# Performance work log

Measured on AMD Instinct MI355X. Metric: run time of the kernel, lower is better.

Reference implementation:

```python
import jax, jax.numpy as jnp
import numpy as np

B = 8
SEQ = 8192
D_MODEL = 256
D_STATE = 64
D_CONV = 4
EXPAND = 4
HEADDIM = 64
N_LAYERS = 8
D_INNER = EXPAND * D_MODEL            # 1024
NHEADS = D_INNER // HEADDIM           # 16
CONV_DIM = D_INNER + 2 * D_STATE      # 1152 (ngroups=1)
D_IN_PROJ = 2 * D_INNER + 2 * D_STATE + NHEADS  # 2192


def setup_inputs():
    key = jax.random.key(0)
    ks = jax.random.split(key, 16)
    rn = lambda k, shape, fan: jax.random.normal(k, shape, jnp.float32) / np.float32(np.sqrt(fan))
    inp = {}
    inp["x"] = jax.random.normal(ks[0], (B, 3, SEQ), jnp.float32)
    inp["conv1_w"] = rn(ks[1], (64, 3, 16), 3 * 16)
    inp["conv1_b"] = rn(ks[2], (64,), 64)
    inp["conv2_w"] = rn(ks[3], (D_MODEL, 64, 16), 64 * 16)
    inp["conv2_b"] = rn(ks[4], (D_MODEL,), D_MODEL)
    inp["in_proj_w"] = rn(ks[5], (N_LAYERS, D_IN_PROJ, D_MODEL), D_MODEL)
    inp["dw_conv_w"] = rn(ks[6], (N_LAYERS, CONV_DIM, D_CONV), D_CONV)
    inp["dw_conv_b"] = rn(ks[7], (N_LAYERS, CONV_DIM), D_CONV)
    inp["dt_bias"] = jax.random.normal(ks[8], (N_LAYERS, NHEADS), jnp.float32) * 0.5
    inp["A_log"] = jax.random.uniform(ks[9], (N_LAYERS, NHEADS), jnp.float32, 0.0, 2.0)
    inp["ssm_D"] = jnp.ones((N_LAYERS, NHEADS), jnp.float32)
    inp["rms_w"] = jnp.ones((N_LAYERS, D_INNER), jnp.float32)
    inp["out_proj_w"] = rn(ks[10], (N_LAYERS, D_MODEL, D_INNER), D_INNER)
    inp["ln_w"] = jnp.ones((D_MODEL,), jnp.float32)
    inp["ln_b"] = jnp.zeros((D_MODEL,), jnp.float32)
    inp["reg1_w"] = rn(ks[11], (128, D_MODEL), D_MODEL)
    inp["reg1_b"] = rn(ks[12], (128,), 128)
    inp["reg2_w"] = rn(ks[13], (1, 128), 128)
    inp["reg2_b"] = rn(ks[14], (1,), 128)
    return inp


def _silu(v):
    return v * jax.nn.sigmoid(v)


def _mamba2_layer(u, in_proj_w, dw_w, dw_b, dt_bias, A_log, ssm_D, rms_w, out_proj_w):
    b, l, _ = u.shape
    zxbcdt = u @ in_proj_w.T                               # (b,l,2192)
    z = zxbcdt[..., :D_INNER]
    xBC = zxbcdt[..., D_INNER:D_INNER + CONV_DIM]
    dt = jax.nn.softplus(zxbcdt[..., D_INNER + CONV_DIM:] + dt_bias)   # (b,l,h)
    # causal depthwise conv1d (kernel D_CONV), then SiLU
    pad = jnp.pad(xBC, ((0, 0), (D_CONV - 1, 0), (0, 0)))
    conv = sum(pad[:, k:k + l, :] * dw_w[:, k] for k in range(D_CONV)) + dw_b
    xBC = _silu(conv)
    xh = xBC[..., :D_INNER].reshape(b, l, NHEADS, HEADDIM)  # (b,l,h,p)
    Bm = xBC[..., D_INNER:D_INNER + D_STATE]                # (b,l,n)
    Cm = xBC[..., D_INNER + D_STATE:]                       # (b,l,n)
    dA = jnp.exp(dt * (-jnp.exp(A_log)))                    # (b,l,h)

    def step(h, inp):
        dA_t, dt_t, x_t, B_t, C_t = inp
        h = h * dA_t[:, :, None, None] + (dt_t[:, :, None] * x_t)[..., None] * B_t[:, None, None, :]
        y = jnp.einsum('bhpn,bn->bhp', h, C_t)
        return h, y

    h0 = jnp.zeros((b, NHEADS, HEADDIM, D_STATE), u.dtype)
    xs = (dA.transpose(1, 0, 2), dt.transpose(1, 0, 2),
          xh.transpose(1, 0, 2, 3), Bm.transpose(1, 0, 2), Cm.transpose(1, 0, 2))
    _, ys = jax.lax.scan(step, h0, xs)                      # (l,b,h,p)
    y = ys.transpose(1, 0, 2, 3) + ssm_D[None, None, :, None] * xh
    y = y.reshape(b, l, D_INNER)
    y = y * _silu(z)                                        # gated
    y = y * jax.lax.rsqrt(jnp.mean(y * y, axis=-1, keepdims=True) + 1e-5) * rms_w
    return y @ out_proj_w.T


def reference(x, conv1_w, conv1_b, conv2_w, conv2_b, in_proj_w, dw_conv_w, dw_conv_b,
              dt_bias, A_log, ssm_D, rms_w, out_proj_w, ln_w, ln_b,
              reg1_w, reg1_b, reg2_w, reg2_b):
    dn = ('NCH', 'OIH', 'NCH')
    h = jax.lax.conv_general_dilated(x, conv1_w, (4,), [(6, 6)], dimension_numbers=dn) + conv1_b[None, :, None]
    h = jax.nn.gelu(h, approximate=False)
    h = jax.lax.conv_general_dilated(h, conv2_w, (2,), [(7, 7)], dimension_numbers=dn) + conv2_b[None, :, None]
    h = jax.nn.gelu(h, approximate=False)
    h = h.transpose(0, 2, 1)                                # (b, 1024, d_model)
    for i in range(N_LAYERS):
        h = _mamba2_layer(h, in_proj_w[i], dw_conv_w[i], dw_conv_b[i],
                          dt_bias[i], A_log[i], ssm_D[i], rms_w[i], out_proj_w[i])
    mu = jnp.mean(h, -1, keepdims=True)
    var = jnp.mean((h - mu) ** 2, -1, keepdims=True)
    h = (h - mu) * jax.lax.rsqrt(var + 1e-5) * ln_w + ln_b  # LayerNorm
    pooled = h.mean(1)
    r = jax.nn.gelu(pooled @ reg1_w.T + reg1_b, approximate=False)
    return r @ reg2_w.T + reg2_b                            # (b, 1)
```

## Files before the change

kernel.cpp:

```cpp
#include <hip/hip_runtime.h>
#include <math.h>

#define NB       8
#define SEQ      8192
#define L1OUT    2048
#define LOUT     1024
#define DMODEL   256
#define DINNER   1024
#define NHEADS   16
#define HEADDIM  64
#define DSTATE   64
#define CONVDIM  1152
#define DINPROJ  2192
#define NPADIN   2304
#define NLAYERS  8
#define NCHUNK   16
#define Q        64

#define N_CAST1 (NLAYERS * NPADIN * DMODEL)
#define N_CAST2 (NLAYERS * DMODEL * DINNER)
#define N_CAST3 (DMODEL * 1024)

typedef _Float16 f16;
typedef __attribute__((ext_vector_type(8))) _Float16 f16x8;
typedef __attribute__((ext_vector_type(4))) _Float16 f16x4;
typedef __attribute__((ext_vector_type(4))) float    f32x4;

__device__ __forceinline__ float gelu_f(float v) {
    return 0.5f * v * (1.0f + erff(v * 0.70710678118654752f));
}
__device__ __forceinline__ float silu_f(float v) {
    return v * __builtin_amdgcn_rcpf(1.0f + __expf(-v));
}

__device__ __forceinline__ void gload16(const void* g, void* l) {
    __builtin_amdgcn_global_load_lds(
        (const __attribute__((address_space(1))) unsigned int*)g,
        (__attribute__((address_space(3))) unsigned int*)l, 16, 0, 0);
}

__device__ __forceinline__ int xcd_chunk(int flat, int nblk) {
    return (flat & 7) * (nblk >> 3) + (flat >> 3);
}

__global__ __launch_bounds__(256) void k_castall(const float* __restrict__ w_in,
                                                 const float* __restrict__ w_out,
                                                 const float* __restrict__ w_c2,
                                                 f16* __restrict__ o_in,
                                                 f16* __restrict__ o_out,
                                                 f16* __restrict__ o_c2) {
    int idx = blockIdx.x * 256 + threadIdx.x;
    if (idx < N_CAST1) {
        int c = idx & 255;
        int r = (idx >> 8) % NPADIN;
        int l = idx / (NPADIN * 256);
        float v = (r < DINPROJ) ? w_in[((size_t)l * DINPROJ + r) * 256 + c] : 0.f;
        o_in[idx] = (f16)v;
    } else if (idx < N_CAST1 + N_CAST2) {
        int i = idx - N_CAST1;
        o_out[i] = (f16)w_out[i];
    } else if (idx < N_CAST1 + N_CAST2 + N_CAST3) {
        int i = idx - N_CAST1 - N_CAST2;
        o_c2[i] = (f16)w_c2[i];
    }
}

__global__ __launch_bounds__(256) void k_conv1(const float* __restrict__ x,
                                               const float* __restrict__ w,
                                               const float* __restrict__ bias,
                                               f16* __restrict__ out) {
    int idx = blockIdx.x * 256 + threadIdx.x;
    int u  = idx & 255;
    int co = (idx >> 8) & 63;
    int b  = idx >> 14;
    int xbase = u * 32 - 8;

    float acc[8];
#pragma unroll
    for (int t = 0; t < 8; ++t) acc[t] = bias[co];

#pragma unroll
    for (int ci = 0; ci < 3; ++ci) {
        const float* xp = x + ((size_t)b * 3 + ci) * SEQ;
        float xb[48];
#pragma unroll
        for (int j = 0; j < 12; ++j) {
            int off = xbase + j * 4;
            float4 v;
            if (off >= 0 && off + 3 < SEQ) {
                v = *(const float4*)&xp[off];
            } else {
                v.x = (off + 0 >= 0 && off + 0 < SEQ) ? xp[off + 0] : 0.f;
                v.y = (off + 1 >= 0 && off + 1 < SEQ) ? xp[off + 1] : 0.f;
                v.z = (off + 2 >= 0 && off + 2 < SEQ) ? xp[off + 2] : 0.f;
                v.w = (off + 3 >= 0 && off + 3 < SEQ) ? xp[off + 3] : 0.f;
            }
            xb[j * 4 + 0] = v.x; xb[j * 4 + 1] = v.y;
            xb[j * 4 + 2] = v.z; xb[j * 4 + 3] = v.w;
        }
        const float* wp = w + (co * 3 + ci) * 16;
        float wv[16];
#pragma unroll
        for (int k = 0; k < 16; ++k) wv[k] = wp[k];
#pragma unroll
        for (int t = 0; t < 8; ++t)
#pragma unroll
            for (int k = 0; k < 16; ++k)
                acc[t] = fmaf(xb[t * 4 + k + 2], wv[k], acc[t]);
    }
    f16x8 o;
#pragma unroll
    for (int t = 0; t < 8; ++t) o[t] = (f16)gelu_f(acc[t]);
    *(f16x8*)&out[((size_t)(b * 64 + co)) * L1OUT + u * 8] = o;
}

__global__ __launch_bounds__(256) void k_im2col(const f16* __restrict__ h1,
                                                f16* __restrict__ A) {
    int idx = blockIdx.x * 256 + threadIdx.x;
    int g = idx & 127;
    int row = idx >> 7;
    int t = row & (LOUT - 1);
    int b = row >> 10;
    int ci = g >> 1, k0 = (g & 1) * 8;
    int pos0 = t * 2 + k0 - 7;
    const f16* hp = h1 + ((size_t)(b * 64 + ci)) * L1OUT;
    f16x8 v;
#pragma unroll
    for (int j = 0; j < 8; ++j) {
        int p = pos0 + j;
        v[j] = (p >= 0 && p < L1OUT) ? hp[p] : (f16)0.f;
    }
    *(f16x8*)&A[(size_t)row * 1024 + g * 8] = v;
}

template<int BM, int EPI>
__global__ __launch_bounds__(256) void k_hgemm(const f16* __restrict__ A,
                                               const f16* __restrict__ Bw,
                                               f16* __restrict__ Ch,
                                               int M, int N, int K,
                                               const float* __restrict__ bias,
                                               const float* __restrict__ dt_bias,
                                               const float* __restrict__ A_log,
                                               float* __restrict__ dadt) {
    constexpr int MI = BM / 32;
    __shared__ f16 As[BM * 64];
    __shared__ f16 Bs[128 * 64];
    int tid  = threadIdx.x;
    int lane = tid & 63, wid = tid >> 6;
    int wm = wid >> 1, wn = wid & 1;

    int nbx = gridDim.x;
    int flat = blockIdx.y * nbx + blockIdx.x;
    int logical = xcd_chunk(flat, nbx * gridDim.y);
    int row0 = (logical / nbx) * BM, col0 = (logical % nbx) * 128;
    int lr = lane & 15, kb = lane >> 4;

    f32x4 acc[MI][4];
#pragma unroll
    for (int mi = 0; mi < MI; ++mi)
#pragma unroll
        for (int ni = 0; ni < 4; ++ni)
            acc[mi][ni] = (f32x4){0.f, 0.f, 0.f, 0.f};

    int sr  = tid >> 3;
    int scx = ((tid & 7) ^ (sr & 7)) * 8;
    int rsw = (lr & 7) * 8;

    for (int k0 = 0; k0 < K; k0 += 64) {
        __syncthreads();
#pragma unroll
        for (int is = 0; is < BM / 32; ++is)
            gload16(A + (size_t)(row0 + is * 32 + sr) * K + k0 + scx,
                    &As[is * 2048 + wid * 512]);
#pragma unroll
        for (int is = 0; is < 4; ++is)
            gload16(Bw + (size_t)(col0 + is * 32 + sr) * K + k0 + scx,
                    &Bs[is * 2048 + wid * 512]);
        __syncthreads();

#pragma unroll
        for (int ks = 0; ks < 2; ++ks) {
            int cbase = (ks * 32 + kb * 8) ^ rsw;
            f16x8 a[MI], b[4];
#pragma unroll
            for (int mi = 0; mi < MI; ++mi)
                a[mi] = *reinterpret_cast<const f16x8*>(
                    &As[(wm * (BM / 2) + mi * 16 + lr) * 64 + cbase]);
#pragma unroll
            for (int ni = 0; ni < 4; ++ni)
                b[ni] = *reinterpret_cast<const f16x8*>(
                    &Bs[(wn * 64 + ni * 16 + lr) * 64 + cbase]);
#pragma unroll
            for (int mi = 0; mi < MI; ++mi)
#pragma unroll
                for (int ni = 0; ni < 4; ++ni)
                    acc[mi][ni] = __builtin_amdgcn_mfma_f32_16x16x32_f16(
                        a[mi], b[ni], acc[mi][ni], 0, 0, 0);
        }
    }

#pragma unroll
    for (int mi = 0; mi < MI; ++mi)
#pragma unroll
        for (int ni = 0; ni < 4; ++ni) {
            int ccol = col0 + wn * 64 + ni * 16 + lr;
            if (ccol < N) {
                int rbase = row0 + wm * (BM / 2) + mi * 16 + kb * 4;
                f32x4 v = acc[mi][ni];
#pragma unroll
                for (int r = 0; r < 4; ++r) {
                    float val = v[r];
                    if (EPI == 1) val = gelu_f(val + bias[ccol]);
                    Ch[(size_t)(rbase + r) * N + ccol] = (f16)val;
                    if (EPI == 2 && ccol >= DINNER + CONVDIM) {
                        int hh = ccol - (DINNER + CONVDIM);
                        float raw = val + dt_bias[hh];
                        float dtv = (raw > 20.f) ? raw : log1pf(__expf(raw));
                        float lda = -__expf(A_log[hh]) * dtv;
                        *(float2*)&dadt[(size_t)(rbase + r) * 32 + hh * 2] =
                            make_float2(lda, dtv);
                    }
                }
            }
        }
}

__global__ __launch_bounds__(256) void k_ssd1(const f16* __restrict__ zx16,
                                              const float* __restrict__ dadt,
                                              const float* __restrict__ dw_w,
                                              const float* __restrict__ dw_b,
                                              const float* __restrict__ ssmD,
                                              f16* __restrict__ y1,
                                              f16* __restrict__ Sbuf16,
                                              float* __restrict__ Abuf,
                                              f16* __restrict__ C16) {
    __shared__ f16 Bs[64][72];
    __shared__ f16 Cs[64][72];
    __shared__ float GT[64][68];
    __shared__ f16 Mw[4][64][72];
    __shared__ float2 LaDt[4][64];

    int tid = threadIdx.x, lane = tid & 63, wid = tid >> 6;
    int bid = xcd_chunk(blockIdx.x, NB * NCHUNK * 4);
    int hq = bid & 3, c = (bid >> 2) & 15, b = bid >> 6;
    int h = hq * 4 + wid;
    int lr = lane & 15, kb = lane >> 4;
    f16* Xs = &Mw[0][0][0];

    {
        int sg = tid % 48;
        int ts = tid / 48;
        if (ts < 4) {
            int xc;
            if (sg < 32)      xc = hq * 256 + sg * 8;
            else if (sg < 40) xc = 1024 + (sg - 32) * 8;
            else              xc = 1088 + (sg - 40) * 8;
            int zc = 1024 + xc;
            float4 wv[8];
            float  bv[8];
#pragma unroll
            for (int j = 0; j < 8; ++j) {
                wv[j] = *(const float4*)&dw_w[(xc + j) * 4];
                bv[j] = dw_b[xc + j];
            }
            int l0 = c * 64 + ts * 16;
            const f16* zrow = zx16 + ((size_t)(b * 1024 + l0)) * DINPROJ + zc;
            f16x8 r0, r1, r2, r3;
            f16x8 zz;
#pragma unroll
            for (int j = 0; j < 8; ++j) zz[j] = (f16)0.f;
            r0 = (l0 >= 3) ? *(const f16x8*)(zrow - 3 * DINPROJ) : zz;
            r1 = (l0 >= 2) ? *(const f16x8*)(zrow - 2 * DINPROJ) : zz;
            r2 = (l0 >= 1) ? *(const f16x8*)(zrow - 1 * DINPROJ) : zz;
#pragma unroll
            for (int t = 0; t < 16; ++t) {
                r3 = *(const f16x8*)(zrow + t * DINPROJ);
                f16x8 o;
#pragma unroll
                for (int j = 0; j < 8; ++j) {
                    float s = bv[j];
                    s = fmaf((float)r0[j], wv[j].x, s);
                    s = fmaf((float)r1[j], wv[j].y, s);
                    s = fmaf((float)r2[j], wv[j].z, s);
                    s = fmaf((float)r3[j], wv[j].w, s);
                    o[j] = (f16)silu_f(s);
                }
                int row = ts * 16 + t;
                if (sg < 32) {
                    f16x4 o0 = {o[0], o[1], o[2], o[3]};
                    f16x4 o1 = {o[4], o[5], o[6], o[7]};
                    *(f16x4*)&Xs[row * 260 + sg * 8]     = o0;
                    *(f16x4*)&Xs[row * 260 + sg * 8 + 4] = o1;
                } else if (sg < 40) {
                    *(f16x8*)&Bs[row][(sg - 32) * 8] = o;
                } else {
                    *(f16x8*)&Cs[row][(sg - 40) * 8] = o;
                }
                r0 = r1; r1 = r2; r2 = r3;
            }
        }
    }

    float2 ad = *(const float2*)&dadt[((size_t)(b * 1024 + c * 64 + lane) * 16 + h) * 2];
    float La = ad.x;
#pragma unroll
    for (int o = 1; o < 64; o <<= 1) {
        float v = __shfl_up(La, o);
        if (lane >= o) La += v;
    }
    float dt_own = ad.y;
    float La63 = __shfl(La, 63);
    float w_own = __expf(La63 - La) * dt_own;
    LaDt[wid][lane] = make_float2(La, dt_own);
    float Dh = ssmD[h];
    __syncthreads();

    if (hq == 0) {
        f16* cp = C16 + (((size_t)(b * 16 + c)) << 12);
#pragma unroll
        for (int it = 0; it < 2; ++it) {
            int cid = it * 256 + tid;
            int row = cid >> 3, off = (cid & 7) * 8;
            *(f16x8*)&cp[row * 64 + off] = *(const f16x8*)&Cs[row][off];
        }
    }

    f16x8 xfrag[4][2];
#pragma unroll
    for (int pi = 0; pi < 4; ++pi)
#pragma unroll
        for (int ks = 0; ks < 2; ++ks) {
            f16x8 v;
#pragma unroll
            for (int j = 0; j < 8; ++j)
                v[j] = Xs[(ks * 32 + kb * 8 + j) * 260 + wid * 64 + pi * 16 + lr];
            xfrag[pi][ks] = v;
        }

    {
        int tq = wid & 1, sq = wid >> 1;
        f32x4 g[2][2];
#pragma unroll
        for (int i = 0; i < 2; ++i)
#pragma unroll
            for (int j = 0; j < 2; ++j) g[i][j] = (f32x4){0.f, 0.f, 0.f, 0.f};
#pragma unroll
        for (int ks = 0; ks < 2; ++ks) {
            f16x8 a[2], bb[2];
#pragma unroll
            for (int ti = 0; ti < 2; ++ti)
                a[ti] = *(const f16x8*)&Cs[tq * 32 + ti * 16 + lr][ks * 32 + kb * 8];
#pragma unroll
            for (int si = 0; si < 2; ++si)
                bb[si] = *(const f16x8*)&Bs[sq * 32 + si * 16 + lr][ks * 32 + kb * 8];
#pragma unroll
            for (int ti = 0; ti < 2; ++ti)
#pragma unroll
                for (int si = 0; si < 2; ++si)
                    g[ti][si] = __builtin_amdgcn_mfma_f32_16x16x32_f16(
                        a[ti], bb[si], g[ti][si], 0, 0, 0);
        }
#pragma unroll
        for (int ti = 0; ti < 2; ++ti)
#pragma unroll
            for (int si = 0; si < 2; ++si)
#pragma unroll
                for (int r = 0; r < 4; ++r)
                    GT[sq * 32 + si * 16 + lr][tq * 32 + ti * 16 + kb * 4 + r] = g[ti][si][r];
    }
    __syncthreads();

    {
        f16x8 brow[8];
#pragma unroll
        for (int i = 0; i < 8; ++i) brow[i] = *(const f16x8*)&Bs[lane][i * 8];
#pragma unroll
        for (int i = 0; i < 8; ++i)
#pragma unroll
            for (int j = 0; j < 8; ++j)
                Mw[wid][i * 8 + j][lane] = (f16)((float)brow[i][j] * w_own);
    }
    __builtin_amdgcn_wave_barrier();

    f16x8 sbfrag[4][2];
#pragma unroll
    for (int ni = 0; ni < 4; ++ni)
#pragma unroll
        for (int ks = 0; ks < 2; ++ks)
            sbfrag[ni][ks] = *(const f16x8*)&Mw[wid][ni * 16 + lr][ks * 32 + kb * 8];

    {
        f32x4 accS[4][4];
#pragma unroll
        for (int pi = 0; pi < 4; ++pi)
#pragma unroll
            for (int ni = 0; ni < 4; ++ni) accS[pi][ni] = (f32x4){0.f, 0.f, 0.f, 0.f};
#pragma unroll
        for (int ks = 0; ks < 2; ++ks)
#pragma unroll
            for (int pi = 0; pi < 4; ++pi)
#pragma unroll
                for (int ni = 0; ni < 4; ++ni)
                    accS[pi][ni] = __builtin_amdgcn_mfma_f32_16x16x32_f16(
                        xfrag[pi][ks], sbfrag[ni][ks], accS[pi][ni], 0, 0, 0);
        size_t sbase = ((size_t)((b * 16 + h) * 16 + c)) << 12;
#pragma unroll
        for (int pi = 0; pi < 4; ++pi)
#pragma unroll
            for (int ni = 0; ni < 4; ++ni)
#pragma unroll
                for (int r = 0; r < 4; ++r)
                    Sbuf16[sbase + (size_t)(pi * 16 + kb * 4 + r) * 64 + ni * 16 + lr] =
                        (f16)accS[pi][ni][r];
        if (lane == 0) Abuf[(b * 16 + h) * 16 + c] = __expf(La63);
    }
    __builtin_amdgcn_wave_barrier();

    {
        int t = lane;
        float la_t = La;
#pragma unroll
        for (int s8 = 0; s8 < 8; ++s8) {
            f16x8 mv;
#pragma unroll
            for (int j = 0; j < 8; ++j) {
                int s = s8 * 8 + j;
                float2 ld = LaDt[wid][s];
                float m = (s <= t) ? GT[s][t] * __expf(la_t - ld.x) * ld.y : 0.f;
                if (s == t) m += Dh;
                mv[j] = (f16)m;
            }
            *(f16x8*)&Mw[wid][t][s8 * 8] = mv;
        }
    }
    __builtin_amdgcn_wave_barrier();

    {
        f32x4 accY[4][4];
#pragma unroll
        for (int ti = 0; ti < 4; ++ti)
#pragma unroll
            for (int pi = 0; pi < 4; ++pi) accY[ti][pi] = (f32x4){0.f, 0.f, 0.f, 0.f};
#pragma unroll
        for (int ks = 0; ks < 2; ++ks) {
            f16x8 af[4];
#pragma unroll
            for (int ti = 0; ti < 4; ++ti)
                af[ti] = *(const f16x8*)&Mw[wid][ti * 16 + lr][ks * 32 + kb * 8];
#pragma unroll
            for (int ti = 0; ti < 4; ++ti)
#pragma unroll
                for (int pi = 0; pi < 4; ++pi)
                    accY[ti][pi] = __builtin_amdgcn_mfma_f32_16x16x32_f16(
                        af[ti], xfrag[pi][ks], accY[ti][pi], 0, 0, 0);
        }
        f16* yp = y1 + ((size_t)(b * 1024 + c * 64)) * 1024 + h * 64;
#pragma unroll
        for (int ti = 0; ti < 4; ++ti)
#pragma unroll
            for (int pi = 0; pi < 4; ++pi)
#pragma unroll
                for (int r = 0; r < 4; ++r)
                    yp[(size_t)(ti * 16 + kb * 4 + r) * 1024 + pi * 16 + lr] =
                        (f16)accY[ti][pi][r];
    }
}

__global__ __launch_bounds__(256) void k_ssd2f(const f16* __restrict__ C16,
                                               const f16* __restrict__ Sbuf16,
                                               const float* __restrict__ Abuf,
                                               const float* __restrict__ dadt,
                                               f16* __restrict__ y2) {
    __shared__ f16 Hs[NCHUNK][1024];
    int tid = threadIdx.x, lane = tid & 63, wv = tid >> 6;
    int bid = xcd_chunk(blockIdx.x, NB * NHEADS * 4);
    int ph = bid & 3, h = (bid >> 2) & 15, b = bid >> 6;
    int bh = b * 16 + h;
    int lr = lane & 15, kb = lane >> 4;
    size_t base = ((size_t)bh << 16) + ph * 1024;

    {
        int lp = tid >> 4;
        int n0 = (tid & 15) * 4;
        int dst = lp * 64 + ((((n0 >> 3) ^ (lp & 7))) << 3) + (n0 & 7);
        float Hl[4];
#pragma unroll
        for (int j = 0; j < 4; ++j) Hl[j] = 0.f;
#pragma unroll
        for (int c = 0; c < NCHUNK; ++c) {
            f16x4 o;
#pragma unroll
            for (int j = 0; j < 4; ++j) o[j] = (f16)Hl[j];
            *(f16x4*)&Hs[c][dst] = o;
            float A = Abuf[bh * 16 + c];
            f16x4 s = *(const f16x4*)&Sbuf16[base + (size_t)c * 4096 + lp * 64 + n0];
#pragma unroll
            for (int j = 0; j < 4; ++j)
                Hl[j] = fmaf(Hl[j], A, (float)s[j]);
        }
    }
    __syncthreads();

    const f16* cpb = C16 + ((size_t)b << 16);
#pragma unroll
    for (int i = 0; i < 4; ++i) {
        int c = wv * 4 + i;
        float2 ad = *(const float2*)&dadt[((size_t)(b * 1024 + c * 64 + lane) * 16 + h) * 2];
        float La = ad.x;
#pragma unroll
        for (int o = 1; o < 64; o <<= 1) {
            float v = __shfl_up(La, o);
            if (lane >= o) La += v;
        }

        f16x8 hfrag[2];
#pragma unroll
        for (int ks = 0; ks < 2; ++ks) {
            int cf = (ks * 32 + kb * 8) ^ ((lr & 7) * 8);
            hfrag[ks] = *(const f16x8*)&Hs[c][lr * 64 + cf];
        }

        const f16* cp = cpb + ((size_t)c << 12);
        f32x4 acc[4];
#pragma unroll
        for (int ti = 0; ti < 4; ++ti) acc[ti] = (f32x4){0.f, 0.f, 0.f, 0.f};
#pragma unroll
        for (int ks = 0; ks < 2; ++ks) {
            f16x8 af[4];
#pragma unroll
            for (int ti = 0; ti < 4; ++ti)
                af[ti] = *(const f16x8*)(cp + (ti * 16 + lr) * 64 + ks * 32 + kb * 8);
#pragma unroll
            for (int ti = 0; ti < 4; ++ti)
                acc[ti] = __builtin_amdgcn_mfma_f32_16x16x32_f16(
                    af[ti], hfrag[ks], acc[ti], 0, 0, 0);
        }
        f16* yp = y2 + ((size_t)(b * 1024 + c * 64)) * 1024 + h * 64 + ph * 16;
#pragma unroll
        for (int ti = 0; ti < 4; ++ti)
#pragma unroll
            for (int r = 0; r < 4; ++r) {
                int t = ti * 16 + kb * 4 + r;
                float sc = __expf(__shfl(La, t));
                yp[(size_t)t * 1024 + lr] = (f16)(sc * acc[ti][r]);
            }
    }
}

__global__ __launch_bounds__(256) void k_gate(const f16* __restrict__ zx16,
                                              const float* __restrict__ rmsw,
                                              const f16* __restrict__ y1,
                                              const f16* __restrict__ y2,
                                              f16* __restrict__ ygate) {
    int tid = threadIdx.x, lane = tid & 63, w = tid >> 6;
    int bl = blockIdx.x * 4 + w;
    int c = lane * 16;
    const f16* p1 = y1 + (size_t)bl * DINNER + c;
    const f16* p2 = y2 + (size_t)bl * DINNER + c;
    const f16* pz = zx16 + (size_t)bl * DINPROJ + c;
    float v[16];
    float ss = 0.f;
#pragma unroll
    for (int hh = 0; hh < 2; ++hh) {
        f16x8 a = *(const f16x8*)(p1 + hh * 8);
        f16x8 b2 = *(const f16x8*)(p2 + hh * 8);
        f16x8 z = *(const f16x8*)(pz + hh * 8);
#pragma unroll
        for (int j = 0; j < 8; ++j) {
            float vv = ((float)a[j] + (float)b2[j]) * silu_f((float)z[j]);
            v[hh * 8 + j] = vv;
            ss += vv * vv;
        }
    }
#pragma unroll
    for (int o = 32; o > 0; o >>= 1) ss += __shfl_xor(ss, o);
    float r = rsqrtf(ss * (1.f / DINNER) + 1e-5f);
#pragma unroll
    for (int hh = 0; hh < 2; ++hh) {
        f16x8 o8;
#pragma unroll
        for (int j = 0; j < 8; ++j)
            o8[j] = (f16)(v[hh * 8 + j] * r * rmsw[c + hh * 8 + j]);
        *(f16x8*)&ygate[(size_t)bl * DINNER + c + hh * 8] = o8;
    }
}

__global__ __launch_bounds__(256) void k_lnpool(const f16* __restrict__ h,
                                                const float* __restrict__ lnw,
                                                const float* __restrict__ lnb,
                                                float* __restrict__ pooledp) {
    __shared__ float pl[4][256];
    int bid = blockIdx.x;
    int b = bid >> 5, seg = bid & 31;
    int tid = threadIdx.x, lane = tid & 63, w = tid >> 6;
    int c4 = lane * 4;
    float4 lw = *(const float4*)&lnw[c4];
    float4 lb = *(const float4*)&lnb[c4];
    float acc0 = 0.f, acc1 = 0.f, acc2 = 0.f, acc3 = 0.f;
    const f16* hb = h + ((size_t)b * 1024 + seg * 32 + w * 8) * DMODEL;
#pragma unroll
    for (int i = 0; i < 8; ++i) {
        f16x4 hv = *(const f16x4*)(hb + (size_t)i * DMODEL + c4);
        float vx = (float)hv.x, vy = (float)hv.y, vz = (float)hv.z, vw = (float)hv.w;
        float s1 = vx + vy + vz + vw;
        float s2 = vx * vx + vy * vy + vz * vz + vw * vw;
#pragma unroll
        for (int o = 32; o > 0; o >>= 1) {
            s1 += __shfl_xor(s1, o);
            s2 += __shfl_xor(s2, o);
        }
        float mu = s1 * (1.f / DMODEL);
        float var = s2 * (1.f / DMODEL) - mu * mu;
        float rr = rsqrtf(var + 1e-5f);
        acc0 += (vx - mu) * rr * lw.x + lb.x;
        acc1 += (vy - mu) * rr * lw.y + lb.y;
        acc2 += (vz - mu) * rr * lw.z + lb.z;
        acc3 += (vw - mu) * rr * lw.w + lb.w;
    }
    pl[w][c4 + 0] = acc0; pl[w][c4 + 1] = acc1;
    pl[w][c4 + 2] = acc2; pl[w][c4 + 3] = acc3;
    __syncthreads();
    float tot = pl[0][tid] + pl[1][tid] + pl[2][tid] + pl[3][tid];
    pooledp[(size_t)(b * 32 + seg) * 256 + tid] = tot;
}

__global__ __launch_bounds__(128) void k_head(const float* __restrict__ pooledp,
                                              const float* __restrict__ w1,
                                              const float* __restrict__ b1,
                                              const float* __restrict__ w2,
                                              const float* __restrict__ b2,
                                              float* __restrict__ out) {
    __shared__ float sp[256];
    __shared__ float red[2];
    int b = blockIdx.x, j = threadIdx.x;
    for (int d = j; d < 256; d += 128) {
        float s = 0.f;
#pragma unroll
        for (int seg = 0; seg < 32; ++seg)
            s += pooledp[(size_t)(b * 32 + seg) * 256 + d];
        sp[d] = s * (1.f / LOUT);
    }
    __syncthreads();
    float acc = b1[j];
#pragma unroll 8
    for (int d = 0; d < DMODEL; ++d)
        acc = fmaf(sp[d], w1[j * DMODEL + d], acc);
    float r = gelu_f(acc) * w2[j];
#pragma unroll
    for (int o = 32; o > 0; o >>= 1) r += __shfl_down(r, o, 64);
    int lane = j & 63, wid = j >> 6;
    if (lane == 0) red[wid] = r;
    __syncthreads();
    if (j == 0) out[b] = red[0] + red[1] + b2[0];
}

extern "C" void kernel_launch(void* const* d_in, const int* in_sizes, int n_in,
                              void* d_out, int out_size, void* d_ws, size_t ws_size,
                              hipStream_t stream) {
    const float* x         = (const float*)d_in[0];
    const float* conv1_w   = (const float*)d_in[1];
    const float* conv1_b   = (const float*)d_in[2];
    const float* conv2_w   = (const float*)d_in[3];
    const float* conv2_b   = (const float*)d_in[4];
    const float* in_proj_w = (const float*)d_in[5];
    const float* dw_w      = (const float*)d_in[6];
    const float* dw_b      = (const float*)d_in[7];
    const float* dt_bias   = (const float*)d_in[8];
    const float* A_log     = (const float*)d_in[9];
    const float* ssm_D     = (const float*)d_in[10];
    const float* rms_w     = (const float*)d_in[11];
    const float* out_proj_w= (const float*)d_in[12];
    const float* ln_w      = (const float*)d_in[13];
    const float* ln_b      = (const float*)d_in[14];
    const float* reg1_w    = (const float*)d_in[15];
    const float* reg1_b    = (const float*)d_in[16];
    const float* reg2_w    = (const float*)d_in[17];
    const float* reg2_b    = (const float*)d_in[18];

    float* ws = (float*)d_ws;
    size_t off = 0;
    float* dadt    = ws + off; off += (size_t)NB * LOUT * NHEADS * 2;
    float* Abuf    = ws + off; off += (size_t)NB * NHEADS * NCHUNK;
    float* pooledp = ws + off; off += (size_t)NB * 32 * 256;

    f16* fbase = (f16*)(ws + off);
    size_t foff = 0;
    f16* c1f16  = fbase + foff; foff += (size_t)NB * 64 * L1OUT;
    f16* hbf0   = fbase + foff; foff += (size_t)NB * LOUT * DMODEL;
    f16* hbf1   = fbase + foff; foff += (size_t)NB * LOUT * DMODEL;
    f16* ygate  = fbase + foff; foff += (size_t)NB * LOUT * DINNER;
    f16* y2     = fbase + foff; foff += (size_t)NB * LOUT * DINNER;
    f16* y1     = fbase + foff; foff += (size_t)NB * LOUT * DINNER;
    f16* C16    = fbase + foff; foff += (size_t)NB * NCHUNK * 64 * 64;
    f16* zx16   = fbase + foff; foff += (size_t)NB * LOUT * DINPROJ;
    f16* Sbuf16 = fbase + foff; foff += (size_t)NB * NHEADS * NCHUNK * 4096;
    f16* w_in_h = fbase + foff; foff += (size_t)NLAYERS * NPADIN * DMODEL;
    f16* w_out_h= fbase + foff; foff += (size_t)NLAYERS * DMODEL * DINNER;
    f16* w_c2_h = fbase + foff; foff += (size_t)DMODEL * 1024;
    f16* im2h   = y1;

    {
        int total = N_CAST1 + N_CAST2 + N_CAST3;
        k_castall<<<(total + 255) / 256, 256, 0, stream>>>(
            in_proj_w, out_proj_w, conv2_w, w_in_h, w_out_h, w_c2_h);
    }

    k_conv1<<<(NB * 64 * 256) / 256, 256, 0, stream>>>(x, conv1_w, conv1_b, c1f16);
    k_im2col<<<(NB * LOUT * 128) / 256, 256, 0, stream>>>(c1f16, im2h);
    {
        dim3 g(256 / 128, 8192 / 64);
        k_hgemm<64, 1><<<g, 256, 0, stream>>>(im2h, w_c2_h, hbf0,
                                              8192, 256, 1024, conv2_b,
                                              nullptr, nullptr, nullptr);
    }

    f16* hcur = hbf0;
    f16* hnxt = hbf1;
    for (int i = 0; i < NLAYERS; ++i) {
        {
            dim3 g(NPADIN / 128, 8192 / 128);
            k_hgemm<128, 2><<<g, 256, 0, stream>>>(
                hcur, w_in_h + (size_t)i * NPADIN * DMODEL, zx16,
                8192, DINPROJ, DMODEL, nullptr,
                dt_bias + i * NHEADS, A_log + i * NHEADS, dadt);
        }
        k_ssd1<<<NB * NCHUNK * 4, 256, 0, stream>>>(
            zx16, dadt, dw_w + (size_t)i * CONVDIM * 4, dw_b + (size_t)i * CONVDIM,
            ssm_D + i * NHEADS, y1, Sbuf16, Abuf, C16);
        k_ssd2f<<<NB * NHEADS * 4, 256, 0, stream>>>(C16, Sbuf16, Abuf, dadt, y2);
        k_gate<<<NB * LOUT / 4, 256, 0, stream>>>(zx16, rms_w + (size_t)i * DINNER,
                                                  y1, y2, ygate);
        {
            dim3 g(DMODEL / 128, 8192 / 64);
            k_hgemm<64, 0><<<g, 256, 0, stream>>>(
                ygate, w_out_h + (size_t)i * DMODEL * DINNER, hnxt,
                8192, DMODEL, DINNER, nullptr, nullptr, nullptr, nullptr);
        }
        f16* tmp = hcur; hcur = hnxt; hnxt = tmp;
    }

    k_lnpool<<<NB * 32, 256, 0, stream>>>(hcur, ln_w, ln_b, pooledp);
    k_head<<<NB, 128, 0, stream>>>(pooledp, reg1_w, reg1_b, reg2_w, reg2_b, (float*)d_out);
}
```

Measured before the change: 856.4 us.

## Fuse gated RMSNorm into out-projection GEMM and fold rms weight into weights

Replaces the separate gating/RMSNorm kernel and out-projection GEMM with a single kernel. Each block computes the gated values for 32 rows in registers, reduces the norm, then runs an MFMA GEMM against the out-projection weights loaded into LDS. The rms weight is folded into the f16 weights during the one-time cast. This removes the ygate round trip through global memory and one launch per layer, but uses 32-row tiles with 256 blocks, lower reuse of the weights, and no overlap between the weight loads and compute.

```diff
diff --git a/kernel.cpp b/kernel.cpp
--- a/kernel.cpp
+++ b/kernel.cpp
@@ -45,6 +45,7 @@
 
 __global__ __launch_bounds__(256) void k_castall(const float* __restrict__ w_in,
                                                  const float* __restrict__ w_out,
+                                                 const float* __restrict__ rmsw,
                                                  const float* __restrict__ w_c2,
                                                  f16* __restrict__ o_in,
                                                  f16* __restrict__ o_out,
@@ -58,7 +59,9 @@
         o_in[idx] = (f16)v;
     } else if (idx < N_CAST1 + N_CAST2) {
         int i = idx - N_CAST1;
-        o_out[i] = (f16)w_out[i];
+        int k = i % DINNER;
+        int l = i / (DMODEL * DINNER);
+        o_out[i] = (f16)(w_out[i] * rmsw[l * DINNER + k]);
     } else if (idx < N_CAST1 + N_CAST2 + N_CAST3) {
         int i = idx - N_CAST1 - N_CAST2;
         o_c2[i] = (f16)w_c2[i];
@@ -547,42 +550,103 @@
     }
 }
 
-__global__ __launch_bounds__(256) void k_gate(const f16* __restrict__ zx16,
-                                              const float* __restrict__ rmsw,
-                                              const f16* __restrict__ y1,
-                                              const f16* __restrict__ y2,
-                                              f16* __restrict__ ygate) {
-    int tid = threadIdx.x, lane = tid & 63, w = tid >> 6;
-    int bl = blockIdx.x * 4 + w;
-    int c = lane * 16;
-    const f16* p1 = y1 + (size_t)bl * DINNER + c;
-    const f16* p2 = y2 + (size_t)bl * DINNER + c;
-    const f16* pz = zx16 + (size_t)bl * DINPROJ + c;
-    float v[16];
+__global__ __launch_bounds__(256) void k_goproj(const f16* __restrict__ y1,
+                                                const f16* __restrict__ y2,
+                                                const f16* __restrict__ zx16,
+                                                const f16* __restrict__ Bw,
+                                                f16* __restrict__ out) {
+    __shared__ f16 Bs[256 * 64];
+    __shared__ f16 Ag[32 * 64];
+    int tid = threadIdx.x, lane = tid & 63, wv = tid >> 6;
+    int row0 = xcd_chunk(blockIdx.x, 256) * 32;
+    int lr = lane & 15, kb = lane >> 4;
+    int row = tid >> 3, seg = tid & 7;
+
+    f16x8 vreg[16];
     float ss = 0.f;
-#pragma unroll
-    for (int hh = 0; hh < 2; ++hh) {
-        f16x8 a = *(const f16x8*)(p1 + hh * 8);
-        f16x8 b2 = *(const f16x8*)(p2 + hh * 8);
-        f16x8 z = *(const f16x8*)(pz + hh * 8);
-#pragma unroll
-        for (int j = 0; j < 8; ++j) {
-            float vv = ((float)a[j] + (float)b2[j]) * silu_f((float)z[j]);
-            v[hh * 8 + j] = vv;
-            ss += vv * vv;
-        }
-    }
-#pragma unroll
-    for (int o = 32; o > 0; o >>= 1) ss += __shfl_xor(ss, o);
-    float r = rsqrtf(ss * (1.f / DINNER) + 1e-5f);
-#pragma unroll
-    for (int hh = 0; hh < 2; ++hh) {
-        f16x8 o8;
-#pragma unroll
-        for (int j = 0; j < 8; ++j)
-            o8[j] = (f16)(v[hh * 8 + j] * r * rmsw[c + hh * 8 + j]);
-        *(f16x8*)&ygate[(size_t)bl * DINNER + c + hh * 8] = o8;
-    }
+    {
+        const f16* p1 = y1 + (size_t)(row0 + row) * DINNER;
+        const f16* p2 = y2 + (size_t)(row0 + row) * DINNER;
+        const f16* pz = zx16 + (size_t)(row0 + row) * DINPROJ;
+#pragma unroll
+        for (int kc = 0; kc < 16; ++kc) {
+            int c = kc * 64 + seg * 8;
+            f16x8 a = *(const f16x8*)(p1 + c);
+            f16x8 b = *(const f16x8*)(p2 + c);
+            f16x8 z = *(const f16x8*)(pz + c);
+            f16x8 o;
+#pragma unroll
+            for (int j = 0; j < 8; ++j) {
+                float v = ((float)a[j] + (float)b[j]) * silu_f((float)z[j]);
+                ss += v * v;
+                o[j] = (f16)v;
+            }
+            vreg[kc] = o;
+        }
+        ss += __shfl_xor(ss, 1);
+        ss += __shfl_xor(ss, 2);
+        ss += __shfl_xor(ss, 4);
+    }
+    float rnorm = rsqrtf(ss * (1.f / DINNER) + 1e-5f);
+
+    int sr  = tid >> 3;
+    int scx = ((tid & 7) ^ (sr & 7)) * 8;
+    int rsw = (lr & 7) * 8;
+    int agw = (seg ^ (row & 7)) * 8;
+
+    f32x4 acc[2][4];
+#pragma unroll
+    for (int mi = 0; mi < 2; ++mi)
+#pragma unroll
+        for (int ni = 0; ni < 4; ++ni)
+            acc[mi][ni] = (f32x4){0.f, 0.f, 0.f, 0.f};
+
+#pragma unroll
+    for (int kc = 0; kc < 16; ++kc) {
+        int k0 = kc * 64;
+        __syncthreads();
+#pragma unroll
+        for (int is = 0; is < 8; ++is)
+            gload16(Bw + (size_t)(is * 32 + sr) * DINNER + k0 + scx,
+                    &Bs[is * 2048 + wv * 512]);
+        {
+            f16x8 o;
+#pragma unroll
+            for (int j = 0; j < 8; ++j)
+                o[j] = (f16)((float)vreg[kc][j] * rnorm);
+            *(f16x8*)&Ag[row * 64 + agw] = o;
+        }
+        __syncthreads();
+
+#pragma unroll
+        for (int ks = 0; ks < 2; ++ks) {
+            int cb = (ks * 32 + kb * 8) ^ rsw;
+            f16x8 a0 = *(const f16x8*)&Ag[lr * 64 + cb];
+            f16x8 a1 = *(const f16x8*)&Ag[(16 + lr) * 64 + cb];
+            f16x8 bfr[4];
+#pragma unroll
+            for (int ni = 0; ni < 4; ++ni)
+                bfr[ni] = *(const f16x8*)&Bs[(wv * 64 + ni * 16 + lr) * 64 + cb];
+#pragma unroll
+            for (int ni = 0; ni < 4; ++ni) {
+                acc[0][ni] = __builtin_amdgcn_mfma_f32_16x16x32_f16(
+                    a0, bfr[ni], acc[0][ni], 0, 0, 0);
+                acc[1][ni] = __builtin_amdgcn_mfma_f32_16x16x32_f16(
+                    a1, bfr[ni], acc[1][ni], 0, 0, 0);
+            }
+        }
+    }
+
+#pragma unroll
+    for (int mi = 0; mi < 2; ++mi)
+#pragma unroll
+        for (int ni = 0; ni < 4; ++ni) {
+            int ccol = wv * 64 + ni * 16 + lr;
+#pragma unroll
+            for (int r = 0; r < 4; ++r)
+                out[(size_t)(row0 + mi * 16 + kb * 4 + r) * DMODEL + ccol] =
+                    (f16)acc[mi][ni][r];
+        }
 }
 
 __global__ __launch_bounds__(256) void k_lnpool(const f16* __restrict__ h,
@@ -688,7 +752,6 @@
     f16* c1f16  = fbase + foff; foff += (size_t)NB * 64 * L1OUT;
     f16* hbf0   = fbase + foff; foff += (size_t)NB * LOUT * DMODEL;
     f16* hbf1   = fbase + foff; foff += (size_t)NB * LOUT * DMODEL;
-    f16* ygate  = fbase + foff; foff += (size_t)NB * LOUT * DINNER;
     f16* y2     = fbase + foff; foff += (size_t)NB * LOUT * DINNER;
     f16* y1     = fbase + foff; foff += (size_t)NB * LOUT * DINNER;
     f16* C16    = fbase + foff; foff += (size_t)NB * NCHUNK * 64 * 64;
@@ -702,7 +765,7 @@
     {
         int total = N_CAST1 + N_CAST2 + N_CAST3;
         k_castall<<<(total + 255) / 256, 256, 0, stream>>>(
-            in_proj_w, out_proj_w, conv2_w, w_in_h, w_out_h, w_c2_h);
+            in_proj_w, out_proj_w, rms_w, conv2_w, w_in_h, w_out_h, w_c2_h);
     }
 
     k_conv1<<<(NB * 64 * 256) / 256, 256, 0, stream>>>(x, conv1_w, conv1_b, c1f16);
@@ -728,14 +791,8 @@
             zx16, dadt, dw_w + (size_t)i * CONVDIM * 4, dw_b + (size_t)i * CONVDIM,
             ssm_D + i * NHEADS, y1, Sbuf16, Abuf, C16);
         k_ssd2f<<<NB * NHEADS * 4, 256, 0, stream>>>(C16, Sbuf16, Abuf, dadt, y2);
-        k_gate<<<NB * LOUT / 4, 256, 0, stream>>>(zx16, rms_w + (size_t)i * DINNER,
-                                                  y1, y2, ygate);
-        {
-            dim3 g(DMODEL / 128, 8192 / 64);
-            k_hgemm<64, 0><<<g, 256, 0, stream>>>(
-                ygate, w_out_h + (size_t)i * DMODEL * DINNER, hnxt,
-                8192, DMODEL, DINNER, nullptr, nullptr, nullptr, nullptr);
-        }
+        k_goproj<<<8192 / 32, 256, 0, stream>>>(
+            y1, y2, zx16, w_out_h + (size_t)i * DMODEL * DINNER, hnxt);
         f16* tmp = hcur; hcur = hnxt; hnxt = tmp;
     }
 
```

Result: faster. 839.5 us (median of 2 runs) (-2.0%).
